# Optimization experiments

Measured on AMD Instinct MI355X. Metric: run time of the kernel, lower is better.

Reference implementation:

```python
import jax, jax.numpy as jnp
import numpy as np

B, CL, QL, D2 = 64, 1024, 128, 512  # batch, c_len, q_len, hidden_size*2


def setup_inputs() -> dict:
    key = jax.random.key(0)
    ks = jax.random.split(key, 6)
    scale = 1.0 / np.sqrt(D2)
    return {
        "c": jax.random.normal(ks[0], (B, CL, D2), jnp.float32),
        "q": jax.random.normal(ks[1], (B, QL, D2), jnp.float32),
        "w_c": jax.random.normal(ks[2], (D2,), jnp.float32) * scale,
        "b_c": jnp.zeros((1,), jnp.float32),
        "w_q": jax.random.normal(ks[3], (D2,), jnp.float32) * scale,
        "b_q": jnp.zeros((1,), jnp.float32),
        "w_cq": jax.random.normal(ks[4], (D2,), jnp.float32) * scale,
        "b_cq": jnp.zeros((1,), jnp.float32),
    }


def reference(c, q, w_c, b_c, w_q, b_q, w_cq, b_cq):
    # BiDAF trilinear similarity.
    # Source loops over q_len: att_weight_cq(c * q_i); equivalent to
    # cq[b,i,j] = sum_d c[b,i,d] * q[b,j,d] * w_cq[d] + b_cq  -> single batched matmul.
    s_c = c @ w_c + b_c  # [B, CL]
    s_q = q @ w_q + b_q  # [B, QL]
    cq = jnp.einsum("bid,bjd->bij", c * w_cq, q) + b_cq  # [B, CL, QL]
    s = s_c[:, :, None] + s_q[:, None, :] + cq  # [B, CL, QL]
    a = jax.nn.softmax(s, axis=2)
    c2q = jnp.einsum("bij,bjd->bid", a, q)  # context-to-query attention
    b_att = jax.nn.softmax(jnp.max(s, axis=2), axis=1)  # [B, CL]
    q2c = jnp.einsum("bi,bid->bd", b_att, c)[:, None, :]  # [B, 1, D2], broadcast over CL
    x = jnp.concatenate([c, c2q, c * c2q, c * q2c], axis=-1)  # [B, CL, 8H]
    return x
```

## Files before the change

kernel.cpp:

```cpp
#include <hip/hip_runtime.h>

using bf16x8 = __attribute__((ext_vector_type(8))) short;
using f32x4  = __attribute__((ext_vector_type(4))) float;

#define NB 64
#define CLN 1024
#define QLN 128
#define DDN 512

typedef __attribute__((address_space(1))) const void GAS;
typedef __attribute__((address_space(3))) void LAS;

__device__ __forceinline__ unsigned f2bf(float x){
    union { float f; unsigned u; } v; v.f = x;
    unsigned r = v.u + 0x7FFFu + ((v.u >> 16) & 1u);
    return r >> 16;
}
__device__ __forceinline__ float bf2f(unsigned short u){
    union { unsigned u; float f; } v; v.u = ((unsigned)u) << 16; return v.f;
}

__global__ __launch_bounds__(256) void k0_qprep(const float* __restrict__ q,
        unsigned short* __restrict__ qT, unsigned short* __restrict__ qbf){
    __shared__ float tile[QLN][65];
    const int b  = blockIdx.x;
    const int d0 = blockIdx.y * 64;
    const int t  = threadIdx.x;
    {
        const int col = t & 63, rg = t >> 6;
        #pragma unroll 4
        for (int p = 0; p < 32; ++p){
            int j = p*4 + rg;
            float v = q[(size_t)(b*QLN + j)*DDN + d0 + col];
            tile[j][col] = v;
            qbf[(size_t)(b*QLN + j)*DDN + d0 + col] = (unsigned short)f2bf(v);
        }
    }
    __syncthreads();
    {
        const int j = t & 127, dg = t >> 7;
        #pragma unroll 4
        for (int p = 0; p < 32; ++p){
            int dd = p*2 + dg;
            qT[(size_t)(b*DDN + d0 + dd)*QLN + j] = (unsigned short)f2bf(tile[j][dd]);
        }
    }
}

__global__ __launch_bounds__(256) void k0b_sq(const float* __restrict__ q,
        const float* __restrict__ w_q, float* __restrict__ sq){
    const int b = blockIdx.x;
    const int t = threadIdx.x;
    const int wave = t >> 6, lane = t & 63;
    float wv[8];
    #pragma unroll
    for (int e=0;e<8;++e) wv[e] = w_q[lane*8+e];
    for (int j = wave; j < QLN; j += 4){
        const float* qr = q + (size_t)(b*QLN + j)*DDN + lane*8;
        float s = 0.f;
        #pragma unroll
        for (int e=0;e<8;++e) s += qr[e]*wv[e];
        #pragma unroll
        for (int m=1;m<64;m<<=1) s += __shfl_xor(s, m, 64);
        if (lane==0) sq[b*QLN + j] = s;
    }
}

__global__ __launch_bounds__(256) void k0c_cprep(const float* __restrict__ c,
        const float* __restrict__ w_c, const float* __restrict__ w_cq,
        float* out, float* __restrict__ sc_ws, float* __restrict__ inv_ws){
    const int t = threadIdx.x, lane = t & 63, w = t >> 6;
    const int row0 = blockIdx.x*32 + w*8;
    float4 wc0 = *(const float4*)(w_c  + lane*8);
    float4 wc1 = *(const float4*)(w_c  + lane*8 + 4);
    float4 wq0 = *(const float4*)(w_cq + lane*8);
    float4 wq1 = *(const float4*)(w_cq + lane*8 + 4);
    #pragma unroll 2
    for (int p=0;p<8;++p){
        const size_t gi = (size_t)(row0 + p);
        const float* cr = c + gi*DDN + lane*8;
        f32x4 a  = *(const f32x4*)cr;
        f32x4 bb = *(const f32x4*)(cr+4);
        float s = a.x*wc0.x + a.y*wc0.y + a.z*wc0.z + a.w*wc0.w
                + bb.x*wc1.x + bb.y*wc1.y + bb.z*wc1.z + bb.w*wc1.w;
        #pragma unroll
        for (int m=1;m<64;m<<=1) s += __shfl_xor(s, m, 64);
        float* orow = out + gi*2048;
        __builtin_nontemporal_store(a,  (f32x4*)(orow + lane*8));
        __builtin_nontemporal_store(bb, (f32x4*)(orow + lane*8 + 4));
        uint4 pk;
        pk.x = f2bf(a.x*wq0.x)  | (f2bf(a.y*wq0.y)  << 16);
        pk.y = f2bf(a.z*wq0.z)  | (f2bf(a.w*wq0.w)  << 16);
        pk.z = f2bf(bb.x*wq1.x) | (f2bf(bb.y*wq1.y) << 16);
        pk.w = f2bf(bb.z*wq1.z) | (f2bf(bb.w*wq1.w) << 16);
        *(uint4*)((unsigned short*)(orow + 1792) + lane*8) = pk;
        if (lane==0) sc_ws[gi] = s;
    }
    if (blockIdx.x == 0){
        for (int d=t; d<DDN; d+=256){
            float wv = w_cq[d];
            inv_ws[d] = (fabsf(wv) > 1e-35f) ? 1.0f/wv : 0.0f;
        }
    }
}

__device__ __forceinline__ void stage_tile(const float* out, size_t girow0, int kc,
        unsigned short* buf, int wm, int lane){
    const int rsub = lane >> 3, c16 = lane & 7;
    #pragma unroll
    for (int r=0;r<4;++r){
        const int chunk = wm*4 + r;
        const int row   = chunk*8 + rsub;
        const int col16 = c16 ^ (row & 7);
        const unsigned short* g =
            (const unsigned short*)(out + (girow0 + row)*2048 + 1792) + kc*64 + col16*8;
        __builtin_amdgcn_global_load_lds((GAS*)g, (LAS*)(buf + chunk*512), 16, 0, 0);
    }
}

__global__ __launch_bounds__(256,3) void k1_main(
        float* out, const unsigned short* __restrict__ qbf,
        const unsigned short* __restrict__ qT, const float* __restrict__ sq_ws,
        const float* __restrict__ sc_ws, const float* __restrict__ inv_ws,
        float* __restrict__ vts, float* __restrict__ Mts, float* __restrict__ Sts){
    __shared__ unsigned short sm_u[16384];
    __shared__ float sm_vw[4][512];
    __shared__ float sm_inv[512];
    __shared__ float sm_sq[128], sm_m[128], sm_wrow[128], sm_sc[128];
    __shared__ float sm_red[8];

    const int bid  = blockIdx.x;
    const int swzb = (bid & 7)*64 + (bid >> 3);
    const int b    = swzb >> 3;
    const int tile = swzb & 7;
    const int i0   = tile * 128;
    const int t    = threadIdx.x;
    const int lane = t & 63;
    const int wm   = t >> 6;
    const int l15  = lane & 15;
    const int l4   = lane >> 4;
    const size_t girow0 = (size_t)(b*CLN + i0);

    if (t < 128){ sm_sc[t] = sc_ws[girow0 + t]; sm_sq[t] = sq_ws[b*QLN + t]; }
    sm_inv[t] = inv_ws[t]; sm_inv[t+256] = inv_ws[t+256];

    f32x4 acc[2][8];
    #pragma unroll
    for (int mi=0;mi<2;++mi)
        #pragma unroll
        for (int nj=0;nj<8;++nj) acc[mi][nj] = f32x4{0.f,0.f,0.f,0.f};

    stage_tile(out, girow0, 0, sm_u, wm, lane);
    __syncthreads();
    const unsigned short* qbbase = qbf + (size_t)b*QLN*DDN;
    for (int kc=0; kc<8; ++kc){
        const int cur = kc & 1;
        if (kc < 7) stage_tile(out, girow0, kc+1, sm_u + (cur^1)*8192, wm, lane);
        const char* abase = (const char*)sm_u + cur*16384;
        #pragma unroll
        for (int ks=0; ks<2; ++ks){
            bf16x8 af[2], bfr[8];
            #pragma unroll
            for (int mi=0;mi<2;++mi){
                const int row = wm*32 + mi*16 + l15;
                af[mi] = *(const bf16x8*)(abase + row*128 + ((ks*64 + l4*16) ^ ((row&7)<<4)));
            }
            #pragma unroll
            for (int nj=0;nj<8;++nj)
                bfr[nj] = *(const bf16x8*)(qbbase + (size_t)(nj*16+l15)*DDN + kc*64 + ks*32 + l4*8);
            #pragma unroll
            for (int mi=0;mi<2;++mi)
                #pragma unroll
                for (int nj=0;nj<8;++nj)
                    acc[mi][nj] = __builtin_amdgcn_mfma_f32_16x16x32_bf16(bfr[nj], af[mi], acc[mi][nj], 0,0,0);
        }
        __syncthreads();
    }

    f32x4 sq4[8];
    #pragma unroll
    for (int nj=0;nj<8;++nj) sq4[nj] = *(const f32x4*)(sm_sq + nj*16 + l4*4);

    #pragma unroll
    for (int mi=0;mi<2;++mi){
        const int irow = wm*32 + mi*16 + l15;
        float rmax = -1e30f;
        #pragma unroll
        for (int nj=0;nj<8;++nj){
            #pragma unroll
            for (int r=0;r<4;++r){
                float v = acc[mi][nj][r] + sq4[nj][r];
                acc[mi][nj][r] = v;
                rmax = fmaxf(rmax, v);
            }
        }
        rmax = fmaxf(rmax, __shfl_xor(rmax, 16, 64));
        rmax = fmaxf(rmax, __shfl_xor(rmax, 32, 64));
        if (l4 == 0) sm_m[irow] = sm_sc[irow] + rmax;
        float rsum = 0.f;
        #pragma unroll
        for (int nj=0;nj<8;++nj){
            #pragma unroll
            for (int r=0;r<4;++r){
                float pv = __expf(acc[mi][nj][r] - rmax);
                acc[mi][nj][r] = pv;
                rsum += pv;
            }
        }
        rsum += __shfl_xor(rsum, 16, 64);
        rsum += __shfl_xor(rsum, 32, 64);
        const float pinv = 1.f / rsum;
        #pragma unroll
        for (int nj=0;nj<8;++nj){
            uint2 u;
            u.x = f2bf(acc[mi][nj][0]*pinv) | (f2bf(acc[mi][nj][1]*pinv) << 16);
            u.y = f2bf(acc[mi][nj][2]*pinv) | (f2bf(acc[mi][nj][3]*pinv) << 16);
            *(uint2*)((char*)sm_u + irow*256 + ((nj*32 + l4*8) ^ ((irow&7)<<4))) = u;
        }
    }
    __syncthreads();

    float v0 = (t < 128) ? sm_m[t] : -1e30f;
    #pragma unroll
    for (int m=1;m<64;m<<=1) v0 = fmaxf(v0, __shfl_xor(v0, m, 64));
    if (lane==0) sm_red[wm] = v0;
    __syncthreads();
    const float mt = fmaxf(sm_red[0], sm_red[1]);
    float ev = (t < 128) ? __expf(sm_m[t] - mt) : 0.f;
    if (t < 128) sm_wrow[t] = ev;
    float es = ev;
    #pragma unroll
    for (int m=1;m<64;m<<=1) es += __shfl_xor(es, m, 64);
    if (lane==0) sm_red[4+wm] = es;
    __syncthreads();
    const float St = sm_red[4]+sm_red[5]+sm_red[6]+sm_red[7];
    float wrow_reg[2];
    wrow_reg[0] = sm_wrow[wm*32 + l15];
    wrow_reg[1] = sm_wrow[wm*32 + 16 + l15];

    const unsigned short* qtbase = qT + (size_t)b*DDN*QLN;
    for (int dc=0; dc<4; ++dc){
        f32x4 acc2[8][2];
        #pragma unroll
        for (int dt=0;dt<8;++dt){ acc2[dt][0] = f32x4{0,0,0,0}; acc2[dt][1] = f32x4{0,0,0,0}; }
        #pragma unroll
        for (int jc=0; jc<4; ++jc){
            bf16x8 b2[2];
            #pragma unroll
            for (int mi=0;mi<2;++mi){
                const int irow = wm*32 + mi*16 + l15;
                b2[mi] = *(const bf16x8*)((char*)sm_u + irow*256 + ((jc*64 + l4*16) ^ ((irow&7)<<4)));
            }
            #pragma unroll
            for (int dt=0;dt<8;++dt){
                bf16x8 a2 = *(const bf16x8*)(qtbase + (size_t)(dc*128 + dt*16 + l15)*QLN + jc*32 + l4*8);
                acc2[dt][0] = __builtin_amdgcn_mfma_f32_16x16x32_bf16(a2, b2[0], acc2[dt][0], 0,0,0);
                acc2[dt][1] = __builtin_amdgcn_mfma_f32_16x16x32_bf16(a2, b2[1], acc2[dt][1], 0,0,0);
            }
        }
        #pragma unroll
        for (int dt=0; dt<8; ++dt){
            const int d0 = dc*128 + dt*16 + l4*4;
            f32x4 iv = *(const f32x4*)(sm_inv + d0);
            f32x4 vp = f32x4{0,0,0,0};
            #pragma unroll
            for (int mi=0; mi<2; ++mi){
                const int irow = wm*32 + mi*16 + l15;
                const size_t gi = girow0 + irow;
                const unsigned short* cb = (const unsigned short*)(out + gi*2048 + 1792) + d0;
                uint2 u = *(const uint2*)cb;
                f32x4 cv;
                cv.x = bf2f((unsigned short)(u.x & 0xffff)) * iv.x;
                cv.y = bf2f((unsigned short)(u.x >> 16))    * iv.y;
                cv.z = bf2f((unsigned short)(u.y & 0xffff)) * iv.z;
                cv.w = bf2f((unsigned short)(u.y >> 16))    * iv.w;
                f32x4 v = acc2[dt][mi];
                float* orow = out + gi*2048;
                __builtin_nontemporal_store(v,  (f32x4*)(orow + 512 + d0));
                f32x4 cq; cq.x=cv.x*v.x; cq.y=cv.y*v.y; cq.z=cv.z*v.z; cq.w=cv.w*v.w;
                __builtin_nontemporal_store(cq, (f32x4*)(orow + 1024 + d0));
                const float w = wrow_reg[mi];
                vp.x += w*cv.x; vp.y += w*cv.y; vp.z += w*cv.z; vp.w += w*cv.w;
            }
            #pragma unroll
            for (int m=1;m<16;m<<=1){
                vp.x += __shfl_xor(vp.x, m, 64); vp.y += __shfl_xor(vp.y, m, 64);
                vp.z += __shfl_xor(vp.z, m, 64); vp.w += __shfl_xor(vp.w, m, 64);
            }
            if (l15 == 0) *(f32x4*)(&sm_vw[wm][d0]) = vp;
        }
    }
    __syncthreads();
    for (int d=t; d<DDN; d+=256){
        float s = sm_vw[0][d] + sm_vw[1][d] + sm_vw[2][d] + sm_vw[3][d];
        vts[(size_t)(b*8 + tile)*DDN + d] = s;
    }
    if (t == 0){ Mts[b*8 + tile] = mt; Sts[b*8 + tile] = St; }
}

__global__ __launch_bounds__(256) void k2_combine(const float* __restrict__ vts,
        const float* __restrict__ Mts, const float* __restrict__ Sts,
        float* __restrict__ q2c){
    const int b = blockIdx.x, t = threadIdx.x;
    float Mt[8]; float M = -1e30f;
    #pragma unroll
    for (int i=0;i<8;++i){ Mt[i] = Mts[b*8+i]; M = fmaxf(M, Mt[i]); }
    float coef[8]; float denom = 0.f;
    #pragma unroll
    for (int i=0;i<8;++i){ coef[i] = __expf(Mt[i]-M); denom += coef[i]*Sts[b*8+i]; }
    const float inv = 1.f/denom;
    for (int d=t; d<DDN; d+=256){
        float s = 0.f;
        #pragma unroll
        for (int i=0;i<8;++i) s += coef[i]*vts[(size_t)(b*8+i)*DDN + d];
        q2c[b*DDN + d] = s*inv;
    }
}

__global__ __launch_bounds__(256) void k3_cq2c(float* out,
        const float* __restrict__ q2c, const float* __restrict__ inv_ws){
    const int t = threadIdx.x;
    const int rloc = t >> 6, ch = t & 63;
    for (int pass=0; pass<8; ++pass){
        const size_t rb = (size_t)blockIdx.x + (size_t)pass*2048;
        const size_t gi = rb*4 + rloc;
        const int b = (int)(gi >> 10);
        const unsigned short* cb = (const unsigned short*)(out + gi*2048 + 1792) + ch*8;
        uint4 raw = *(const uint4*)cb;
        const float* qp = q2c + b*DDN + ch*8;
        float4 qa = *(const float4*)qp;
        float4 qb = *(const float4*)(qp+4);
        const float* ip = inv_ws + ch*8;
        float4 ia = *(const float4*)ip;
        float4 ib = *(const float4*)(ip+4);
        f32x4 o0, o1;
        o0.x = bf2f((unsigned short)(raw.x & 0xffff)) * ia.x * qa.x;
        o0.y = bf2f((unsigned short)(raw.x >> 16))    * ia.y * qa.y;
        o0.z = bf2f((unsigned short)(raw.y & 0xffff)) * ia.z * qa.z;
        o0.w = bf2f((unsigned short)(raw.y >> 16))    * ia.w * qa.w;
        o1.x = bf2f((unsigned short)(raw.z & 0xffff)) * ib.x * qb.x;
        o1.y = bf2f((unsigned short)(raw.z >> 16))    * ib.y * qb.y;
        o1.z = bf2f((unsigned short)(raw.w & 0xffff)) * ib.z * qb.z;
        o1.w = bf2f((unsigned short)(raw.w >> 16))    * ib.w * qb.w;
        __syncthreads();
        f32x4* wp = (f32x4*)(out + gi*2048 + 1536) + ch*2;
        __builtin_nontemporal_store(o0, wp);
        __builtin_nontemporal_store(o1, wp+1);
    }
}

extern "C" void kernel_launch(void* const* d_in, const int* in_sizes, int n_in,
                              void* d_out, int out_size, void* d_ws, size_t ws_size,
                              hipStream_t stream) {
    const float* c    = (const float*)d_in[0];
    const float* q    = (const float*)d_in[1];
    const float* w_c  = (const float*)d_in[2];
    const float* w_q  = (const float*)d_in[4];
    const float* w_cq = (const float*)d_in[6];
    float* out = (float*)d_out;

    char* ws = (char*)d_ws;
    unsigned short* qT  = (unsigned short*)ws;
    unsigned short* qbf = (unsigned short*)(ws + 8388608);
    float* sq  = (float*)(ws + 16777216);
    float* sc  = (float*)(ws + 16777216 + 32768);
    float* inv = (float*)(ws + 16777216 + 32768 + 262144);
    float* Mts = (float*)(ws + 16777216 + 32768 + 262144 + 2048);
    float* Sts = (float*)(ws + 16777216 + 32768 + 262144 + 4096);
    float* vts = (float*)(ws + 16777216 + 32768 + 262144 + 6144);
    float* q2c = (float*)(ws + 16777216 + 32768 + 262144 + 6144 + 1048576);

    k0_qprep<<<dim3(NB, 8), 256, 0, stream>>>(q, qT, qbf);
    k0b_sq<<<NB, 256, 0, stream>>>(q, w_q, sq);
    k0c_cprep<<<2048, 256, 0, stream>>>(c, w_c, w_cq, out, sc, inv);
    k1_main<<<NB*8, 256, 0, stream>>>(out, qbf, qT, sq, sc, inv, vts, Mts, Sts);
    k2_combine<<<NB, 256, 0, stream>>>(vts, Mts, Sts, q2c);
    k3_cq2c<<<2048, 256, 0, stream>>>(out, q2c, inv);
}
```

Measured before the change: 280.1 us.

## Split attention kernel into two GEMM kernels with probabilities staged in global memory

The fused main kernel is split into a first kernel that computes scores, softmax probabilities and per-tile max/sum statistics, and a second kernel that does the probability-times-q GEMM and writes the c2q outputs. The probabilities and row weights go through a new global workspace instead of staying in LDS. The first GEMM now loads A fragments directly from global memory instead of staging them into LDS with async copies and a double buffer. This cuts LDS use and barriers, which may raise occupancy, at the cost of an extra launch and an extra global write and read of the probability matrix.

Result: slower. 289.6 us (+3.4%).

```diff
diff --git a/kernel.cpp b/kernel.cpp
--- a/kernel.cpp
+++ b/kernel.cpp
@@ -7,9 +7,6 @@
 #define CLN 1024
 #define QLN 128
 #define DDN 512
-
-typedef __attribute__((address_space(1))) const void GAS;
-typedef __attribute__((address_space(3))) void LAS;
 
 __device__ __forceinline__ unsigned f2bf(float x){
     union { float f; unsigned u; } v; v.f = x;
@@ -104,30 +101,12 @@
     }
 }
 
-__device__ __forceinline__ void stage_tile(const float* out, size_t girow0, int kc,
-        unsigned short* buf, int wm, int lane){
-    const int rsub = lane >> 3, c16 = lane & 7;
-    #pragma unroll
-    for (int r=0;r<4;++r){
-        const int chunk = wm*4 + r;
-        const int row   = chunk*8 + rsub;
-        const int col16 = c16 ^ (row & 7);
-        const unsigned short* g =
-            (const unsigned short*)(out + (girow0 + row)*2048 + 1792) + kc*64 + col16*8;
-        __builtin_amdgcn_global_load_lds((GAS*)g, (LAS*)(buf + chunk*512), 16, 0, 0);
-    }
-}
-
-__global__ __launch_bounds__(256,3) void k1_main(
-        float* out, const unsigned short* __restrict__ qbf,
-        const unsigned short* __restrict__ qT, const float* __restrict__ sq_ws,
-        const float* __restrict__ sc_ws, const float* __restrict__ inv_ws,
-        float* __restrict__ vts, float* __restrict__ Mts, float* __restrict__ Sts){
-    __shared__ unsigned short sm_u[16384];
-    __shared__ float sm_vw[4][512];
-    __shared__ float sm_inv[512];
-    __shared__ float sm_sq[128], sm_m[128], sm_wrow[128], sm_sc[128];
-    __shared__ float sm_red[8];
+__global__ __launch_bounds__(256) void k1a_gemm1(
+        const float* out, const unsigned short* __restrict__ qbf,
+        const float* __restrict__ sq_ws, const float* __restrict__ sc_ws,
+        unsigned short* __restrict__ Pws, float* __restrict__ wrow_ws,
+        float* __restrict__ Mts, float* __restrict__ Sts){
+    __shared__ float sm_sq[128], sm_sc[128], sm_m[128], sm_red[8];
 
     const int bid  = blockIdx.x;
     const int swzb = (bid & 7)*64 + (bid >> 3);
@@ -142,7 +121,7 @@
     const size_t girow0 = (size_t)(b*CLN + i0);
 
     if (t < 128){ sm_sc[t] = sc_ws[girow0 + t]; sm_sq[t] = sq_ws[b*QLN + t]; }
-    sm_inv[t] = inv_ws[t]; sm_inv[t+256] = inv_ws[t+256];
+    __syncthreads();
 
     f32x4 acc[2][8];
     #pragma unroll
@@ -150,37 +129,33 @@
         #pragma unroll
         for (int nj=0;nj<8;++nj) acc[mi][nj] = f32x4{0.f,0.f,0.f,0.f};
 
-    stage_tile(out, girow0, 0, sm_u, wm, lane);
-    __syncthreads();
     const unsigned short* qbbase = qbf + (size_t)b*QLN*DDN;
+    const unsigned short* cb0 = (const unsigned short*)(out + (girow0 + wm*32 + l15)*2048) + 3584;
+    const unsigned short* cb1 = (const unsigned short*)(out + (girow0 + wm*32 + 16 + l15)*2048) + 3584;
+    #pragma unroll 2
     for (int kc=0; kc<8; ++kc){
-        const int cur = kc & 1;
-        if (kc < 7) stage_tile(out, girow0, kc+1, sm_u + (cur^1)*8192, wm, lane);
-        const char* abase = (const char*)sm_u + cur*16384;
         #pragma unroll
         for (int ks=0; ks<2; ++ks){
+            const int koff = kc*64 + ks*32 + l4*8;
             bf16x8 af[2], bfr[8];
-            #pragma unroll
-            for (int mi=0;mi<2;++mi){
-                const int row = wm*32 + mi*16 + l15;
-                af[mi] = *(const bf16x8*)(abase + row*128 + ((ks*64 + l4*16) ^ ((row&7)<<4)));
-            }
+            af[0] = *(const bf16x8*)(cb0 + koff);
+            af[1] = *(const bf16x8*)(cb1 + koff);
             #pragma unroll
             for (int nj=0;nj<8;++nj)
-                bfr[nj] = *(const bf16x8*)(qbbase + (size_t)(nj*16+l15)*DDN + kc*64 + ks*32 + l4*8);
+                bfr[nj] = *(const bf16x8*)(qbbase + (size_t)(nj*16+l15)*DDN + koff);
             #pragma unroll
             for (int mi=0;mi<2;++mi)
                 #pragma unroll
                 for (int nj=0;nj<8;++nj)
                     acc[mi][nj] = __builtin_amdgcn_mfma_f32_16x16x32_bf16(bfr[nj], af[mi], acc[mi][nj], 0,0,0);
         }
-        __syncthreads();
     }
 
     f32x4 sq4[8];
     #pragma unroll
     for (int nj=0;nj<8;++nj) sq4[nj] = *(const f32x4*)(sm_sq + nj*16 + l4*4);
 
+    unsigned short* pbase = Pws + (size_t)(b*8 + tile)*128*128;
     #pragma unroll
     for (int mi=0;mi<2;++mi){
         const int irow = wm*32 + mi*16 + l15;
@@ -215,7 +190,7 @@
             uint2 u;
             u.x = f2bf(acc[mi][nj][0]*pinv) | (f2bf(acc[mi][nj][1]*pinv) << 16);
             u.y = f2bf(acc[mi][nj][2]*pinv) | (f2bf(acc[mi][nj][3]*pinv) << 16);
-            *(uint2*)((char*)sm_u + irow*256 + ((nj*32 + l4*8) ^ ((irow&7)<<4))) = u;
+            *(uint2*)(pbase + irow*128 + nj*16 + l4*4) = u;
         }
     }
     __syncthreads();
@@ -227,17 +202,45 @@
     __syncthreads();
     const float mt = fmaxf(sm_red[0], sm_red[1]);
     float ev = (t < 128) ? __expf(sm_m[t] - mt) : 0.f;
-    if (t < 128) sm_wrow[t] = ev;
+    if (t < 128) wrow_ws[girow0 + t] = ev;
     float es = ev;
     #pragma unroll
     for (int m=1;m<64;m<<=1) es += __shfl_xor(es, m, 64);
     if (lane==0) sm_red[4+wm] = es;
     __syncthreads();
-    const float St = sm_red[4]+sm_red[5]+sm_red[6]+sm_red[7];
+    if (t == 0){
+        Mts[b*8 + tile] = mt;
+        Sts[b*8 + tile] = sm_red[4]+sm_red[5]+sm_red[6]+sm_red[7];
+    }
+}
+
+__global__ __launch_bounds__(256) void k1b_gemm2(
+        float* out, const unsigned short* __restrict__ Pws,
+        const unsigned short* __restrict__ qT, const float* __restrict__ wrow_ws,
+        const float* __restrict__ inv_ws, float* __restrict__ vts){
+    __shared__ float sm_vw[4][512];
+    __shared__ float sm_inv[512];
+
+    const int bid  = blockIdx.x;
+    const int swzb = (bid & 7)*64 + (bid >> 3);
+    const int b    = swzb >> 3;
+    const int tile = swzb & 7;
+    const int i0   = tile * 128;
+    const int t    = threadIdx.x;
+    const int lane = t & 63;
+    const int wm   = t >> 6;
+    const int l15  = lane & 15;
+    const int l4   = lane >> 4;
+    const size_t girow0 = (size_t)(b*CLN + i0);
+
+    sm_inv[t] = inv_ws[t]; sm_inv[t+256] = inv_ws[t+256];
+    __syncthreads();
+
     float wrow_reg[2];
-    wrow_reg[0] = sm_wrow[wm*32 + l15];
-    wrow_reg[1] = sm_wrow[wm*32 + 16 + l15];
-
+    wrow_reg[0] = wrow_ws[girow0 + wm*32 + l15];
+    wrow_reg[1] = wrow_ws[girow0 + wm*32 + 16 + l15];
+
+    const unsigned short* pbase  = Pws + (size_t)(b*8 + tile)*128*128;
     const unsigned short* qtbase = qT + (size_t)b*DDN*QLN;
     for (int dc=0; dc<4; ++dc){
         f32x4 acc2[8][2];
@@ -249,7 +252,7 @@
             #pragma unroll
             for (int mi=0;mi<2;++mi){
                 const int irow = wm*32 + mi*16 + l15;
-                b2[mi] = *(const bf16x8*)((char*)sm_u + irow*256 + ((jc*64 + l4*16) ^ ((irow&7)<<4)));
+                b2[mi] = *(const bf16x8*)(pbase + irow*128 + jc*32 + l4*8);
             }
             #pragma unroll
             for (int dt=0;dt<8;++dt){
@@ -295,7 +298,6 @@
         float s = sm_vw[0][d] + sm_vw[1][d] + sm_vw[2][d] + sm_vw[3][d];
         vts[(size_t)(b*8 + tile)*DDN + d] = s;
     }
-    if (t == 0){ Mts[b*8 + tile] = mt; Sts[b*8 + tile] = St; }
 }
 
 __global__ __launch_bounds__(256) void k2_combine(const float* __restrict__ vts,
@@ -362,18 +364,22 @@
     char* ws = (char*)d_ws;
     unsigned short* qT  = (unsigned short*)ws;
     unsigned short* qbf = (unsigned short*)(ws + 8388608);
-    float* sq  = (float*)(ws + 16777216);
-    float* sc  = (float*)(ws + 16777216 + 32768);
-    float* inv = (float*)(ws + 16777216 + 32768 + 262144);
-    float* Mts = (float*)(ws + 16777216 + 32768 + 262144 + 2048);
-    float* Sts = (float*)(ws + 16777216 + 32768 + 262144 + 4096);
-    float* vts = (float*)(ws + 16777216 + 32768 + 262144 + 6144);
-    float* q2c = (float*)(ws + 16777216 + 32768 + 262144 + 6144 + 1048576);
+    unsigned short* Pws = (unsigned short*)(ws + 16777216);
+    char* ws2 = ws + 33554432;
+    float* sq   = (float*)(ws2);
+    float* sc   = (float*)(ws2 + 32768);
+    float* inv  = (float*)(ws2 + 32768 + 262144);
+    float* Mts  = (float*)(ws2 + 32768 + 262144 + 2048);
+    float* Sts  = (float*)(ws2 + 32768 + 262144 + 4096);
+    float* vts  = (float*)(ws2 + 32768 + 262144 + 6144);
+    float* q2c  = (float*)(ws2 + 32768 + 262144 + 6144 + 1048576);
+    float* wrow = (float*)(ws2 + 32768 + 262144 + 6144 + 1048576 + 131072);
 
     k0_qprep<<<dim3(NB, 8), 256, 0, stream>>>(q, qT, qbf);
     k0b_sq<<<NB, 256, 0, stream>>>(q, w_q, sq);
     k0c_cprep<<<2048, 256, 0, stream>>>(c, w_c, w_cq, out, sc, inv);
-    k1_main<<<NB*8, 256, 0, stream>>>(out, qbf, qT, sq, sc, inv, vts, Mts, Sts);
+    k1a_gemm1<<<NB*8, 256, 0, stream>>>(out, qbf, sq, sc, Pws, wrow, Mts, Sts);
+    k1b_gemm2<<<NB*8, 256, 0, stream>>>(out, Pws, qT, wrow, inv, vts);
     k2_combine<<<NB, 256, 0, stream>>>(vts, Mts, Sts, q2c);
     k3_cq2c<<<2048, 256, 0, stream>>>(out, q2c, inv);
 }
```
